# Performance work log

Hardware: AMD Instinct MI355X
Metric: run time of the kernel (lower is better)

The kernel has to match this reference:

```python
import jax, jax.numpy as jnp
import numpy as np

D = 1024      # d_model
H = 16        # n_head
DH = D // H   # d_head = 64
DFF = 4 * D   # 4096
B, T = 1, 4096
EPS = 1e-5


def _layernorm(x, scale, bias):
    mu = jnp.mean(x, axis=-1, keepdims=True)
    var = jnp.mean(jnp.square(x - mu), axis=-1, keepdims=True)
    return (x - mu) * jax.lax.rsqrt(var + EPS) * scale + bias


def setup_inputs() -> dict:
    key = jax.random.key(0)
    ks = jax.random.split(key, 8)
    s = 0.02
    return {
        "x": jax.random.normal(ks[0], (B, T, D), jnp.float32),
        "ln1_scale": jnp.ones((D,), jnp.float32),
        "ln1_bias": jnp.zeros((D,), jnp.float32),
        "W_attn": jax.random.normal(ks[1], (D, 3 * D), jnp.float32) * s,
        "b_attn": jnp.zeros((3 * D,), jnp.float32),
        "W_proj": jax.random.normal(ks[2], (D, D), jnp.float32) * s,
        "b_proj": jnp.zeros((D,), jnp.float32),
        "ln2_scale": jnp.ones((D,), jnp.float32),
        "ln2_bias": jnp.zeros((D,), jnp.float32),
        "W_fc": jax.random.normal(ks[3], (D, DFF), jnp.float32) * s,
        "b_fc": jnp.zeros((DFF,), jnp.float32),
        "W_fc2": jax.random.normal(ks[4], (DFF, D), jnp.float32) * s,
        "b_fc2": jnp.zeros((D,), jnp.float32),
    }


def reference(x, ln1_scale, ln1_bias, W_attn, b_attn, W_proj, b_proj,
              ln2_scale, ln2_bias, W_fc, b_fc, W_fc2, b_fc2):
    Bx, Tx, C = x.shape
    # --- attention branch ---
    h = _layernorm(x, ln1_scale, ln1_bias)
    qkv = h @ W_attn + b_attn                      # [B,T,3D]
    q, k, v = jnp.split(qkv, 3, axis=-1)
    q = q.reshape(Bx, Tx, H, DH).transpose(0, 2, 1, 3)  # [B,H,T,dh]
    k = k.reshape(Bx, Tx, H, DH).transpose(0, 2, 1, 3)
    v = v.reshape(Bx, Tx, H, DH).transpose(0, 2, 1, 3)
    att = jnp.einsum('bhqd,bhkd->bhqk', q, k) * (1.0 / jnp.sqrt(DH))
    causal = jnp.tril(jnp.ones((Tx, Tx), dtype=jnp.bool_))[None, None]
    att = jnp.where(causal, att, -jnp.inf)
    att = jax.nn.softmax(att, axis=-1)
    y = jnp.einsum('bhqk,bhkd->bhqd', att, v)      # [B,H,T,dh]
    y = y.transpose(0, 2, 1, 3).reshape(Bx, Tx, C)
    y = y @ W_proj + b_proj
    x = x + y
    # --- MLP branch ---
    h2 = _layernorm(x, ln2_scale, ln2_bias)
    m = jax.nn.gelu(h2 @ W_fc + b_fc)              # approximate gelu (flax default)
    m = m @ W_fc2 + b_fc2
    return x + m
```

## Files before the change

kernel.cpp:

```cpp
#include <hip/hip_runtime.h>
#include <hip/hip_bf16.h>

typedef short bf16x8 __attribute__((ext_vector_type(8)));
typedef float f32x4 __attribute__((ext_vector_type(4)));
typedef unsigned short u16;
typedef unsigned int u32;

#define TSEQ 4096
#define DMODEL 1024
#define NHEAD 16
#define DHEAD 64
#define DFF 4096

__device__ __forceinline__ u16 f2bf(float f) {
    u32 u = __builtin_bit_cast(u32, f);
    u32 lsb = (u >> 16) & 1u;
    u += 0x7fffu + lsb;
    return (u16)(u >> 16);
}

__device__ __forceinline__ float exp2_hw(float x) {
    float r;
    asm("v_exp_f32 %0, %1" : "=v"(r) : "v"(x));
    return r;
}

__device__ __forceinline__ float rcp_hw(float x) {
    float r;
    asm("v_rcp_f32 %0, %1" : "=v"(r) : "v"(x));
    return r;
}

__device__ __forceinline__ u32 cvt_pk_bf16(float a, float b) {
    u32 r;
    asm("v_cvt_pk_bf16_f32 %0, %1, %2" : "=v"(r) : "v"(a), "v"(b));
    return r;
}

__device__ __forceinline__ void gload_lds16(const u16* g, u16* l) {
    __builtin_amdgcn_global_load_lds(
        (const __attribute__((address_space(1))) u32*)g,
        (__attribute__((address_space(3))) u32*)l, 16, 0, 0);
}

__global__ __launch_bounds__(256)
void transpose_cast_kernel(const float* __restrict__ W, u16* __restrict__ Wt, int K, int N)
{
    __shared__ float tile[64][65];
    const int t = threadIdx.x;
    const int c = t & 63, r4 = t >> 6;
    const int col0 = blockIdx.x * 64;
    const int row0 = blockIdx.y * 64;
#pragma unroll
    for (int p = 0; p < 16; p++) {
        const int r = 4 * p + r4;
        tile[r][c] = W[(size_t)(row0 + r) * N + col0 + c];
    }
    __syncthreads();
#pragma unroll
    for (int p = 0; p < 16; p++) {
        const int r = 4 * p + r4;
        Wt[(size_t)(col0 + r) * K + row0 + c] = f2bf(tile[c][r]);
    }
}

__global__ __launch_bounds__(256)
void v_transpose_kernel(const u16* __restrict__ qkv, u16* __restrict__ Vtg)
{
    __shared__ u16 tile[64][72];
    const int t = threadIdx.x;
    const int hh = blockIdx.y, t0 = blockIdx.x * 64;
#pragma unroll
    for (int p = 0; p < 2; p++) {
        const int L = p * 2048 + t * 8;
        const int r = L >> 6, c = L & 63;
        const bf16x8 v = *(const bf16x8*)(qkv + (size_t)(t0 + r) * 3072 + 2048 + hh * 64 + c);
#pragma unroll
        for (int i = 0; i < 8; i++) tile[c + i][r] = (u16)v[i];
    }
    __syncthreads();
#pragma unroll
    for (int p = 0; p < 2; p++) {
        const int L = p * 2048 + t * 8;
        const int d = L >> 6, c = L & 63;
        bf16x8 v;
#pragma unroll
        for (int i = 0; i < 8; i++) v[i] = (short)tile[d][c + i];
        *(bf16x8*)(Vtg + (size_t)(hh * 64 + d) * TSEQ + t0 + c) = v;
    }
}

__global__ __launch_bounds__(256)
void ln_kernel(const float* __restrict__ x, const float* __restrict__ sc,
               const float* __restrict__ bi, u16* __restrict__ out)
{
    const int lane = threadIdx.x & 63;
    const int row = blockIdx.x * 4 + (threadIdx.x >> 6);
    const float* xr = x + (size_t)row * DMODEL;
    float4 v[4];
    float s = 0.f, s2 = 0.f;
#pragma unroll
    for (int q = 0; q < 4; q++) {
        v[q] = *(const float4*)(xr + 4 * (lane + 64 * q));
        s  += v[q].x + v[q].y + v[q].z + v[q].w;
        s2 += v[q].x * v[q].x + v[q].y * v[q].y + v[q].z * v[q].z + v[q].w * v[q].w;
    }
#pragma unroll
    for (int off = 1; off < 64; off <<= 1) {
        s  += __shfl_xor(s, off);
        s2 += __shfl_xor(s2, off);
    }
    const float mu = s * (1.f / DMODEL);
    const float rstd = rsqrtf(s2 * (1.f / DMODEL) - mu * mu + 1e-5f);
#pragma unroll
    for (int q = 0; q < 4; q++) {
        const int c = 4 * (lane + 64 * q);
        const float4 scv = *(const float4*)(sc + c);
        const float4 biv = *(const float4*)(bi + c);
        ushort4 ov;
        ov.x = f2bf((v[q].x - mu) * rstd * scv.x + biv.x);
        ov.y = f2bf((v[q].y - mu) * rstd * scv.y + biv.y);
        ov.z = f2bf((v[q].z - mu) * rstd * scv.z + biv.z);
        ov.w = f2bf((v[q].w - mu) * rstd * scv.w + biv.w);
        *(ushort4*)(out + (size_t)row * DMODEL + c) = ov;
    }
}

template<int BN, int GELU_F, int OUT_BF16, int HAS_RES, int HAS_BIAS>
__global__ __launch_bounds__(256)
void gemm_kernel(const u16* __restrict__ A, int lda,
                 const u16* __restrict__ Bt, int ldb,
                 const float* __restrict__ bias, const float* __restrict__ res,
                 u16* __restrict__ outb, float* __restrict__ outf0,
                 float* __restrict__ outf1, int M, int N, int Kblk)
{
    constexpr int MI = (BN == 128) ? 4 : 2;
    __shared__ u16 Alds[128 * 64];
    __shared__ u16 Blds[BN * 64];
    const int t = threadIdx.x;
    const int lane = t & 63, w = t >> 6;
    const int g = lane >> 4, fr = lane & 15;
    const int m0 = blockIdx.y * 128, n0 = blockIdx.x * BN;
    const size_t koff = (size_t)blockIdx.z * Kblk;
    const int rowbase = (BN == 128) ? (w >> 1) * 64 : w * 32;
    const int colbase = (BN == 128) ? (w & 1) * 64 : 0;
    float* outf = blockIdx.z ? outf1 : outf0;

    f32x4 zero4 = {0.f, 0.f, 0.f, 0.f};
    f32x4 acc[MI][4];
#pragma unroll
    for (int i = 0; i < MI; i++)
#pragma unroll
        for (int j = 0; j < 4; j++) acc[i][j] = zero4;

    for (int k0 = 0; k0 < Kblk; k0 += 64) {
        __syncthreads();
#pragma unroll
        for (int p = 0; p < 4; p++) {
            const int c = p * 256 + t;
            const int r = c >> 3, j = (c & 7) ^ (r & 7);
            gload_lds16(A + (size_t)(m0 + r) * lda + koff + k0 + j * 8, Alds + c * 8);
        }
#pragma unroll
        for (int p = 0; p < (BN == 128 ? 4 : 2); p++) {
            const int c = p * 256 + t;
            const int r = c >> 3, j = (c & 7) ^ (r & 7);
            gload_lds16(Bt + (size_t)(n0 + r) * ldb + koff + k0 + j * 8, Blds + c * 8);
        }
        __syncthreads();

#pragma unroll
        for (int ks = 0; ks < 2; ks++) {
            bf16x8 af[MI], bfr[4];
#pragma unroll
            for (int i = 0; i < MI; i++)
                af[i] = *(const bf16x8*)(Alds + (rowbase + i * 16 + fr) * 64 + (((ks * 4 + g) ^ (fr & 7)) * 8));
#pragma unroll
            for (int j = 0; j < 4; j++)
                bfr[j] = *(const bf16x8*)(Blds + (colbase + j * 16 + fr) * 64 + (((ks * 4 + g) ^ (fr & 7)) * 8));
#pragma unroll
            for (int i = 0; i < MI; i++)
#pragma unroll
                for (int j = 0; j < 4; j++)
                    acc[i][j] = __builtin_amdgcn_mfma_f32_16x16x32_bf16(af[i], bfr[j], acc[i][j], 0, 0, 0);
        }
    }

#pragma unroll
    for (int j = 0; j < 4; j++) {
        const int col = n0 + colbase + j * 16 + fr;
        float bv = 0.f;
        if (HAS_BIAS) bv = bias[col];
#pragma unroll
        for (int i = 0; i < MI; i++) {
#pragma unroll
            for (int r = 0; r < 4; r++) {
                const int row = m0 + rowbase + i * 16 + g * 4 + r;
                float v = acc[i][j][r] + bv;
                if (GELU_F) {
                    const float q = 0.7978845608028654f * (v + 0.044715f * v * v * v);
                    const float e = exp2_hw(fminf(q, 30.f) * 2.8853900817779268f);
                    v = v * e * rcp_hw(e + 1.0f);
                }
                if (HAS_RES) v += res[(size_t)row * N + col];
                if (OUT_BF16) outb[(size_t)row * N + col] = f2bf(v);
                else          outf[(size_t)row * N + col] = v;
            }
        }
    }
}

__global__ __launch_bounds__(256)
void fc2_merge_kernel(float* __restrict__ out, const float* __restrict__ part,
                      const float* __restrict__ x1, const float* __restrict__ bias)
{
    const int i = blockIdx.x * 256 + threadIdx.x;
    const float4 o = ((const float4*)out)[i];
    const float4 p = ((const float4*)part)[i];
    const float4 r = ((const float4*)x1)[i];
    const float4 b = ((const float4*)bias)[i & 255];
    float4 v;
    v.x = o.x + p.x + r.x + b.x;
    v.y = o.y + p.y + r.y + b.y;
    v.z = o.z + p.z + r.z + b.z;
    v.w = o.w + p.w + r.w + b.w;
    ((float4*)out)[i] = v;
}

__device__ __forceinline__ void softmax_update(
    const f32x4 st[4], bool diag, int klim, int g, int fr,
    float& mrow, float& lrow, f32x4 o[4], u16* Pl)
{
    const float ninf = -__builtin_inff();
    const float C = 0.125f * 1.4426950408889634f;
    float av[4][4];
#pragma unroll
    for (int ct = 0; ct < 4; ct++)
#pragma unroll
        for (int r = 0; r < 4; r++) {
            float aa = st[ct][r];
            if (diag && (ct * 16 + g * 4 + r) > klim) aa = ninf;
            av[ct][r] = aa;
        }
    float m0 = fmaxf(fmaxf(av[0][0], av[0][1]), fmaxf(av[0][2], av[0][3]));
    float m1 = fmaxf(fmaxf(av[1][0], av[1][1]), fmaxf(av[1][2], av[1][3]));
    float m2 = fmaxf(fmaxf(av[2][0], av[2][1]), fmaxf(av[2][2], av[2][3]));
    float m3 = fmaxf(fmaxf(av[3][0], av[3][1]), fmaxf(av[3][2], av[3][3]));
    float vm = fmaxf(fmaxf(m0, m1), fmaxf(m2, m3));
    vm = fmaxf(vm, __shfl_xor(vm, 16));
    vm = fmaxf(vm, __shfl_xor(vm, 32));
    const float mn = (vm <= mrow + 64.f) ? mrow : vm;
    const float mnC = mn * C;
    float rs = 0.f;
#pragma unroll
    for (int ct = 0; ct < 4; ct++) {
        const float p0 = exp2_hw(__builtin_fmaf(av[ct][0], C, -mnC));
        const float p1 = exp2_hw(__builtin_fmaf(av[ct][1], C, -mnC));
        const float p2 = exp2_hw(__builtin_fmaf(av[ct][2], C, -mnC));
        const float p3 = exp2_hw(__builtin_fmaf(av[ct][3], C, -mnC));
        rs += (p0 + p1) + (p2 + p3);
        uint2 pk;
        pk.x = cvt_pk_bf16(p0, p1);
        pk.y = cvt_pk_bf16(p2, p3);
        const int chunk = ct * 2 + (g >> 1);
        const int addr = fr * 64 + ((chunk ^ (fr & 7)) * 8) + (g & 1) * 4;
        *(uint2*)(Pl + addr) = pk;
    }
    rs += __shfl_xor(rs, 16);
    rs += __shfl_xor(rs, 32);
    const float sc = exp2_hw((mrow - mn) * C);
    lrow = __builtin_fmaf(lrow, sc, rs);
    const bool nores = (mn == mrow);
    mrow = mn;
    if (!__all(nores)) {
        float scb[4];
#pragma unroll
        for (int j = 0; j < 4; j++) scb[j] = __shfl(sc, g * 4 + j);
#pragma unroll
        for (int dt = 0; dt < 4; dt++)
#pragma unroll
            for (int j = 0; j < 4; j++) o[dt][j] *= scb[j];
    }
}

__global__ __launch_bounds__(512, 4)
void attn_kernel(const u16* __restrict__ qkv, const u16* __restrict__ Vtg,
                 u16* __restrict__ y)
{
    __shared__ u16 Klds[2][128 * 64];
    __shared__ u16 Vlds[2][64 * 128];
    __shared__ u16 Plds[8][16 * 64];
    const int t = threadIdx.x, lane = t & 63, w = t >> 6;
    const int g = lane >> 4, fr = lane & 15;
    const int wv = w & 3, grp = w >> 2;
    const int hh = blockIdx.y;
    const int ii = blockIdx.x;
    const int ntB = 64 - ii;
    const int qAw = ii * 64 + wv * 16;
    const int qBw = (63 - ii) * 64 + wv * 16;

    bf16x8 aqA[2], aqB[2];
#pragma unroll
    for (int s = 0; s < 2; s++) {
        aqA[s] = *(const bf16x8*)(qkv + (size_t)(qAw + fr) * 3072 + hh * 64 + s * 32 + g * 8);
        aqB[s] = *(const bf16x8*)(qkv + (size_t)(qBw + fr) * 3072 + hh * 64 + s * 32 + g * 8);
    }

    f32x4 zero4 = {0.f, 0.f, 0.f, 0.f};
    f32x4 oA[4] = {zero4, zero4, zero4, zero4};
    f32x4 oB[4] = {zero4, zero4, zero4, zero4};
    const float ninf = -__builtin_inff();
    float mA = ninf, lA = 0.f, mB = ninf, lB = 0.f;

    const int cK0 = t, cK1 = t + 512;
    const int rK0 = cK0 >> 3, jK0 = (cK0 & 7) ^ (rK0 & 7);
    const int rK1 = cK1 >> 3, jK1 = (cK1 & 7) ^ (rK1 & 7);
    const int rv0 = cK0 >> 4, cj0 = cK0 & 15;
    const int jv0 = (cj0 & 8) | ((cj0 & 7) ^ (rv0 & 7));
    const int rv1 = cK1 >> 4, cj1 = cK1 & 15;
    const int jv1 = (cj1 & 8) | ((cj1 & 7) ^ (rv1 & 7));
    const u16* gk0 = qkv + (size_t)rK0 * 3072 + 1024 + hh * 64 + jK0 * 8;
    const u16* gk1 = qkv + (size_t)rK1 * 3072 + 1024 + hh * 64 + jK1 * 8;
    const u16* gv0 = Vtg + (size_t)(hh * 64 + rv0) * TSEQ + jv0 * 8;
    const u16* gv1 = Vtg + (size_t)(hh * 64 + rv1) * TSEQ + jv1 * 8;

#define STAGE(buf, k0) do { \
        gload_lds16(gk0 + (size_t)(k0) * 3072, Klds[buf] + cK0 * 8); \
        gload_lds16(gk1 + (size_t)(k0) * 3072, Klds[buf] + cK1 * 8); \
        gload_lds16(gv0 + (k0), Vlds[buf] + cK0 * 8); \
        gload_lds16(gv1 + (k0), Vlds[buf] + cK1 * 8); \
    } while (0)

    const int nIter = (65 - ii) >> 1;
    STAGE(0, 0);

    int cur = 0;
    for (int j = 0; j < nIter; j++) {
        __syncthreads();
        if (j + 1 < nIter) STAGE(cur ^ 1, (j + 1) * 128);

        const int kt = 2 * j + grp;
        const bool aB = kt < ntB;
        const bool aA = kt <= ii;
        if (aB | aA) {
            const u16* Kl = Klds[cur] + grp * (64 * 64);
            const u16* Vl = Vlds[cur];
            const int klim = wv * 16 + fr;

            f32x4 stA[4] = {zero4, zero4, zero4, zero4};
            f32x4 stB[4] = {zero4, zero4, zero4, zero4};
#pragma unroll
            for (int ct = 0; ct < 4; ct++) {
#pragma unroll
                for (int ds = 0; ds < 2; ds++) {
                    const bf16x8 bk = *(const bf16x8*)(Kl + (ct * 16 + fr) * 64 + (((ds * 4 + g) ^ (fr & 7)) * 8));
                    if (aB) stB[ct] = __builtin_amdgcn_mfma_f32_16x16x32_bf16(bk, aqB[ds], stB[ct], 0, 0, 0);
                    if (aA) stA[ct] = __builtin_amdgcn_mfma_f32_16x16x32_bf16(bk, aqA[ds], stA[ct], 0, 0, 0);
                }
            }

            if (aB) {
                softmax_update(stB, kt == ntB - 1, klim, g, fr, mB, lB, oB, Plds[w]);
                __builtin_amdgcn_s_waitcnt(0xc07f);
#pragma unroll
                for (int kkh = 0; kkh < 2; kkh++) {
                    const bf16x8 pa = *(const bf16x8*)(&Plds[w][fr * 64 + (((kkh * 4 + g) ^ (fr & 7)) * 8)]);
#pragma unroll
                    for (int dt = 0; dt < 4; dt++) {
                        const int cc = grp * 8 + kkh * 4 + g;
                        const bf16x8 bv = *(const bf16x8*)(Vl + (dt * 16 + fr) * 128 + (((cc & 8) | ((cc & 7) ^ (fr & 7))) * 8));
                        oB[dt] = __builtin_amdgcn_mfma_f32_16x16x32_bf16(pa, bv, oB[dt], 0, 0, 0);
                    }
                }
            }
            if (aA) {
                softmax_update(stA, kt == ii, klim, g, fr, mA, lA, oA, Plds[w]);
                __builtin_amdgcn_s_waitcnt(0xc07f);
#pragma unroll
                for (int kkh = 0; kkh < 2; kkh++) {
                    const bf16x8 pa = *(const bf16x8*)(&Plds[w][fr * 64 + (((kkh * 4 + g) ^ (fr & 7)) * 8)]);
#pragma unroll
                    for (int dt = 0; dt < 4; dt++) {
                        const int cc = grp * 8 + kkh * 4 + g;
                        const bf16x8 bv = *(const bf16x8*)(Vl + (dt * 16 + fr) * 128 + (((cc & 8) | ((cc & 7) ^ (fr & 7))) * 8));
                        oA[dt] = __builtin_amdgcn_mfma_f32_16x16x32_bf16(pa, bv, oA[dt], 0, 0, 0);
                    }
                }
            }
        }
        cur ^= 1;
    }
#undef STAGE

    __syncthreads();
    float* Of = (float*)&Klds[0][0];
    float2* Ml = (float2*)&Vlds[0][0];
    const float C = 0.125f * 1.4426950408889634f;
    if (grp == 1) {
#pragma unroll
        for (int dt = 0; dt < 4; dt++)
#pragma unroll
            for (int jq = 0; jq < 4; jq++) {
                Of[((wv * 2 + 0) * 16 + g * 4 + jq) * 64 + dt * 16 + fr] = oA[dt][jq];
                Of[((wv * 2 + 1) * 16 + g * 4 + jq) * 64 + dt * 16 + fr] = oB[dt][jq];
            }
        if (g == 0) {
            Ml[(wv * 2 + 0) * 16 + fr] = make_float2(mA, lA);
            Ml[(wv * 2 + 1) * 16 + fr] = make_float2(mB, lB);
        }
    }
    __syncthreads();
    if (grp == 0) {
#pragma unroll
        for (int jq = 0; jq < 4; jq++) {
            {
                const float m0 = __shfl(mA, g * 4 + jq), l0 = __shfl(lA, g * 4 + jq);
                const float2 ml1 = Ml[(wv * 2 + 0) * 16 + g * 4 + jq];
                const float mm = fmaxf(m0, ml1.x);
                const float s0 = exp2_hw((m0 - mm) * C);
                const float s1 = exp2_hw((ml1.x - mm) * C);
                const float rl = rcp_hw(__builtin_fmaf(l0, s0, ml1.y * s1));
#pragma unroll
                for (int dt = 0; dt < 4; dt++) {
                    const float o1 = Of[((wv * 2 + 0) * 16 + g * 4 + jq) * 64 + dt * 16 + fr];
                    y[(size_t)(qAw + g * 4 + jq) * DMODEL + hh * 64 + dt * 16 + fr] =
                        f2bf((oA[dt][jq] * s0 + o1 * s1) * rl);
                }
            }
            {
                const float m0 = __shfl(mB, g * 4 + jq), l0 = __shfl(lB, g * 4 + jq);
                const float2 ml1 = Ml[(wv * 2 + 1) * 16 + g * 4 + jq];
                const float mm = fmaxf(m0, ml1.x);
                const float s0 = exp2_hw((m0 - mm) * C);
                const float s1 = exp2_hw((ml1.x - mm) * C);
                const float rl = rcp_hw(__builtin_fmaf(l0, s0, ml1.y * s1));
#pragma unroll
                for (int dt = 0; dt < 4; dt++) {
                    const float o1 = Of[((wv * 2 + 1) * 16 + g * 4 + jq) * 64 + dt * 16 + fr];
                    y[(size_t)(qBw + g * 4 + jq) * DMODEL + hh * 64 + dt * 16 + fr] =
                        f2bf((oB[dt][jq] * s0 + o1 * s1) * rl);
                }
            }
        }
    }
}

extern "C" void kernel_launch(void* const* d_in, const int* in_sizes, int n_in,
                              void* d_out, int out_size, void* d_ws, size_t ws_size,
                              hipStream_t stream)
{
    const float* x      = (const float*)d_in[0];
    const float* ln1_s  = (const float*)d_in[1];
    const float* ln1_b  = (const float*)d_in[2];
    const float* W_attn = (const float*)d_in[3];
    const float* b_attn = (const float*)d_in[4];
    const float* W_proj = (const float*)d_in[5];
    const float* b_proj = (const float*)d_in[6];
    const float* ln2_s  = (const float*)d_in[7];
    const float* ln2_b  = (const float*)d_in[8];
    const float* W_fc   = (const float*)d_in[9];
    const float* b_fc   = (const float*)d_in[10];
    const float* W_fc2  = (const float*)d_in[11];
    const float* b_fc2  = (const float*)d_in[12];
    float* out = (float*)d_out;

    char* ws = (char*)d_ws;
    u16* WtAttn = (u16*)ws; ws += (size_t)3072 * 1024 * 2;
    u16* WtProj = (u16*)ws; ws += (size_t)1024 * 1024 * 2;
    u16* WtFc   = (u16*)ws; ws += (size_t)4096 * 1024 * 2;
    u16* WtFc2  = (u16*)ws; ws += (size_t)1024 * 4096 * 2;
    u16* bufA   = (u16*)ws; ws += (size_t)4096 * 1024 * 2;
    u16* bufB   = (u16*)ws; ws += (size_t)4096 * 4096 * 2;
    float* x1   = (float*)ws; ws += (size_t)4096 * 1024 * 4;
    u16* Vtg    = (u16*)x1;
    float* P0   = (float*)d_ws;

    transpose_cast_kernel<<<dim3(3072 / 64, 1024 / 64), 256, 0, stream>>>(W_attn, WtAttn, 1024, 3072);
    transpose_cast_kernel<<<dim3(1024 / 64, 1024 / 64), 256, 0, stream>>>(W_proj, WtProj, 1024, 1024);
    transpose_cast_kernel<<<dim3(4096 / 64, 1024 / 64), 256, 0, stream>>>(W_fc,   WtFc,   1024, 4096);
    transpose_cast_kernel<<<dim3(1024 / 64, 4096 / 64), 256, 0, stream>>>(W_fc2,  WtFc2,  4096, 1024);

    ln_kernel<<<TSEQ / 4, 256, 0, stream>>>(x, ln1_s, ln1_b, bufA);
    gemm_kernel<128, 0, 1, 0, 1><<<dim3(24, 32, 1), 256, 0, stream>>>(
        bufA, 1024, WtAttn, 1024, b_attn, nullptr, bufB, nullptr, nullptr, 4096, 3072, 1024);
    v_transpose_kernel<<<dim3(TSEQ / 64, NHEAD), 256, 0, stream>>>(bufB, Vtg);
    attn_kernel<<<dim3(32, NHEAD), 512, 0, stream>>>(bufB, Vtg, bufA);
    gemm_kernel<64, 0, 0, 1, 1><<<dim3(16, 32, 1), 256, 0, stream>>>(
        bufA, 1024, WtProj, 1024, b_proj, x, nullptr, x1, nullptr, 4096, 1024, 1024);

    ln_kernel<<<TSEQ / 4, 256, 0, stream>>>(x1, ln2_s, ln2_b, bufA);
    gemm_kernel<128, 1, 1, 0, 1><<<dim3(32, 32, 1), 256, 0, stream>>>(
        bufA, 1024, WtFc, 1024, b_fc, nullptr, bufB, nullptr, nullptr, 4096, 4096, 1024);
    gemm_kernel<128, 0, 0, 0, 0><<<dim3(8, 32, 2), 256, 0, stream>>>(
        bufB, 4096, WtFc2, 4096, nullptr, nullptr, nullptr, P0, out, 4096, 1024, 2048);
    fc2_merge_kernel<<<4096, 256, 0, stream>>>(out, P0, x1, b_fc2);
}
```

Baseline: 289.3 us.

## Single-buffer attention K/V tiles for occupancy; fold fc2 bias and residual into GEMM

The attention kernel drops its double-buffered K/V shared-memory staging in favor of a single buffer loaded between two barriers, and raises the launch-bounds occupancy hint from 4 to 6. The intent is to cut LDS use per block so more blocks fit per CU, at the cost of losing the overlap between global loads and compute. The split-K fc2 GEMM now adds bias and residual in its z=1 slice, so the merge kernel reads only two arrays instead of four.

```diff
diff --git a/kernel.cpp b/kernel.cpp
--- a/kernel.cpp
+++ b/kernel.cpp
@@ -126,7 +126,7 @@
     }
 }
 
-template<int BN, int GELU_F, int OUT_BF16, int HAS_RES, int HAS_BIAS>
+template<int BN, int GELU_F, int OUT_BF16, int HAS_RES, int HAS_BIAS, int FUSE_Z1 = 0>
 __global__ __launch_bounds__(256)
 void gemm_kernel(const u16* __restrict__ A, int lda,
                  const u16* __restrict__ Bt, int ldb,
@@ -186,11 +186,13 @@
         }
     }
 
+    const bool fuse = FUSE_Z1 && (blockIdx.z == 1);
 #pragma unroll
     for (int j = 0; j < 4; j++) {
         const int col = n0 + colbase + j * 16 + fr;
         float bv = 0.f;
         if (HAS_BIAS) bv = bias[col];
+        if (FUSE_Z1 && fuse) bv = bias[col];
 #pragma unroll
         for (int i = 0; i < MI; i++) {
 #pragma unroll
@@ -203,6 +205,7 @@
                     v = v * e * rcp_hw(e + 1.0f);
                 }
                 if (HAS_RES) v += res[(size_t)row * N + col];
+                if (FUSE_Z1 && fuse) v += res[(size_t)row * N + col];
                 if (OUT_BF16) outb[(size_t)row * N + col] = f2bf(v);
                 else          outf[(size_t)row * N + col] = v;
             }
@@ -211,19 +214,16 @@
 }
 
 __global__ __launch_bounds__(256)
-void fc2_merge_kernel(float* __restrict__ out, const float* __restrict__ part,
-                      const float* __restrict__ x1, const float* __restrict__ bias)
+void fc2_merge_kernel(float* __restrict__ out, const float* __restrict__ part)
 {
     const int i = blockIdx.x * 256 + threadIdx.x;
     const float4 o = ((const float4*)out)[i];
     const float4 p = ((const float4*)part)[i];
-    const float4 r = ((const float4*)x1)[i];
-    const float4 b = ((const float4*)bias)[i & 255];
     float4 v;
-    v.x = o.x + p.x + r.x + b.x;
-    v.y = o.y + p.y + r.y + b.y;
-    v.z = o.z + p.z + r.z + b.z;
-    v.w = o.w + p.w + r.w + b.w;
+    v.x = o.x + p.x;
+    v.y = o.y + p.y;
+    v.z = o.z + p.z;
+    v.w = o.w + p.w;
     ((float4*)out)[i] = v;
 }
 
@@ -283,16 +283,18 @@
     }
 }
 
-__global__ __launch_bounds__(512, 4)
+__global__ __launch_bounds__(512, 6)
 void attn_kernel(const u16* __restrict__ qkv, const u16* __restrict__ Vtg,
                  u16* __restrict__ y)
 {
-    __shared__ u16 Klds[2][128 * 64];
-    __shared__ u16 Vlds[2][64 * 128];
-    __shared__ u16 Plds[8][16 * 64];
+    __shared__ __align__(16) u16 SMEM[24576];
+    u16* Klds = SMEM;
+    u16* Vlds = SMEM + 128 * 64;
+    u16* Pbase = SMEM + 2 * 128 * 64;
     const int t = threadIdx.x, lane = t & 63, w = t >> 6;
     const int g = lane >> 4, fr = lane & 15;
     const int wv = w & 3, grp = w >> 2;
+    u16* Pl = Pbase + w * (16 * 64);
     const int hh = blockIdx.y;
     const int ii = blockIdx.x;
     const int ntB = 64 - ii;
@@ -324,27 +326,22 @@
     const u16* gv0 = Vtg + (size_t)(hh * 64 + rv0) * TSEQ + jv0 * 8;
     const u16* gv1 = Vtg + (size_t)(hh * 64 + rv1) * TSEQ + jv1 * 8;
 
-#define STAGE(buf, k0) do { \
-        gload_lds16(gk0 + (size_t)(k0) * 3072, Klds[buf] + cK0 * 8); \
-        gload_lds16(gk1 + (size_t)(k0) * 3072, Klds[buf] + cK1 * 8); \
-        gload_lds16(gv0 + (k0), Vlds[buf] + cK0 * 8); \
-        gload_lds16(gv1 + (k0), Vlds[buf] + cK1 * 8); \
-    } while (0)
-
     const int nIter = (65 - ii) >> 1;
-    STAGE(0, 0);
-
-    int cur = 0;
     for (int j = 0; j < nIter; j++) {
+        const int k0 = j * 128;
         __syncthreads();
-        if (j + 1 < nIter) STAGE(cur ^ 1, (j + 1) * 128);
+        gload_lds16(gk0 + (size_t)k0 * 3072, Klds + cK0 * 8);
+        gload_lds16(gk1 + (size_t)k0 * 3072, Klds + cK1 * 8);
+        gload_lds16(gv0 + k0, Vlds + cK0 * 8);
+        gload_lds16(gv1 + k0, Vlds + cK1 * 8);
+        __syncthreads();
 
         const int kt = 2 * j + grp;
         const bool aB = kt < ntB;
         const bool aA = kt <= ii;
         if (aB | aA) {
-            const u16* Kl = Klds[cur] + grp * (64 * 64);
-            const u16* Vl = Vlds[cur];
+            const u16* Kl = Klds + grp * (64 * 64);
+            const u16* Vl = Vlds;
             const int klim = wv * 16 + fr;
 
             f32x4 stA[4] = {zero4, zero4, zero4, zero4};
@@ -360,11 +357,11 @@
             }
 
             if (aB) {
-                softmax_update(stB, kt == ntB - 1, klim, g, fr, mB, lB, oB, Plds[w]);
+                softmax_update(stB, kt == ntB - 1, klim, g, fr, mB, lB, oB, Pl);
                 __builtin_amdgcn_s_waitcnt(0xc07f);
 #pragma unroll
                 for (int kkh = 0; kkh < 2; kkh++) {
-                    const bf16x8 pa = *(const bf16x8*)(&Plds[w][fr * 64 + (((kkh * 4 + g) ^ (fr & 7)) * 8)]);
+                    const bf16x8 pa = *(const bf16x8*)(Pl + fr * 64 + (((kkh * 4 + g) ^ (fr & 7)) * 8));
 #pragma unroll
                     for (int dt = 0; dt < 4; dt++) {
                         const int cc = grp * 8 + kkh * 4 + g;
@@ -374,11 +371,11 @@
                 }
             }
             if (aA) {
-                softmax_update(stA, kt == ii, klim, g, fr, mA, lA, oA, Plds[w]);
+                softmax_update(stA, kt == ii, klim, g, fr, mA, lA, oA, Pl);
                 __builtin_amdgcn_s_waitcnt(0xc07f);
 #pragma unroll
                 for (int kkh = 0; kkh < 2; kkh++) {
-                    const bf16x8 pa = *(const bf16x8*)(&Plds[w][fr * 64 + (((kkh * 4 + g) ^ (fr & 7)) * 8)]);
+                    const bf16x8 pa = *(const bf16x8*)(Pl + fr * 64 + (((kkh * 4 + g) ^ (fr & 7)) * 8));
 #pragma unroll
                     for (int dt = 0; dt < 4; dt++) {
                         const int cc = grp * 8 + kkh * 4 + g;
@@ -388,13 +385,11 @@
                 }
             }
         }
-        cur ^= 1;
-    }
-#undef STAGE
+    }
 
     __syncthreads();
-    float* Of = (float*)&Klds[0][0];
-    float2* Ml = (float2*)&Vlds[0][0];
+    float* Of = (float*)SMEM;
+    float2* Ml = (float2*)Pbase;
     const float C = 0.125f * 1.4426950408889634f;
     if (grp == 1) {
 #pragma unroll
@@ -491,7 +486,7 @@
     ln_kernel<<<TSEQ / 4, 256, 0, stream>>>(x1, ln2_s, ln2_b, bufA);
     gemm_kernel<128, 1, 1, 0, 1><<<dim3(32, 32, 1), 256, 0, stream>>>(
         bufA, 1024, WtFc, 1024, b_fc, nullptr, bufB, nullptr, nullptr, 4096, 4096, 1024);
-    gemm_kernel<128, 0, 0, 0, 0><<<dim3(8, 32, 2), 256, 0, stream>>>(
-        bufB, 4096, WtFc2, 4096, nullptr, nullptr, nullptr, P0, out, 4096, 1024, 2048);
-    fc2_merge_kernel<<<4096, 256, 0, stream>>>(out, P0, x1, b_fc2);
-}
+    gemm_kernel<128, 0, 0, 0, 0, 1><<<dim3(8, 32, 2), 256, 0, stream>>>(
+        bufB, 4096, WtFc2, 4096, b_fc2, x1, nullptr, P0, out, 4096, 1024, 2048);
+    fc2_merge_kernel<<<4096, 256, 0, stream>>>(out, P0);
+}
```

After: 579.2 us. 2x slower.
